# Optimization experiments

Hardware: AMD Instinct MI355X
Metric: run time of the kernel (lower is better)

## Reference

```python
import jax, jax.numpy as jnp
import numpy as np
from functools import partial

C = 10   # number of regular-repr fields
G = 4    # C4 rotation group order
EPS = 1e-5


def _lift_kernel(w):
    """Lifting (trivial->regular) P4 kernel. w: [C, Cin, k, k] ->
    full kernel [C*G, Cin, k, k] with output channel layout (field, orientation)."""
    ks = [jnp.rot90(w, r, axes=(-2, -1)) for r in range(G)]  # each [C,Cin,k,k]
    k = jnp.stack(ks, axis=1)                                 # [C,G,Cin,k,k]
    return k.reshape(w.shape[0] * G, w.shape[1], w.shape[2], w.shape[3])


def _gconv_kernel(w):
    """Regular->regular P4 kernel. w: [Cout, Cin, G, k, k] (indexed by relative
    input orientation) -> full kernel [Cout*G, Cin*G, k, k].
    K[co*G+r, ci*G+s] = rot90(w[co, ci, (s-r) mod G], r)."""
    Cout, Cin, _, k1, k2 = w.shape
    ks = []
    for r in range(G):
        wr = jnp.roll(w, shift=r, axis=2)             # wr[..., s, :, :] = w[..., (s-r)%G]
        wr = jnp.rot90(wr, r, axes=(-2, -1))          # rotate spatially by r*90deg
        ks.append(wr)
    k = jnp.stack(ks, axis=1)                          # [Cout, G, Cin, G, k, k]
    return k.reshape(Cout * G, Cin * G, k1, k2)


def _conv(x, k, pad):
    return jax.lax.conv_general_dilated(
        x, k, window_strides=(1, 1), padding=pad,
        dimension_numbers=('NCHW', 'OIHW', 'NCHW'))


def _bn_relu(x, gamma, beta):
    """InnerBatchNorm (stats shared over the G orientations of each field) + ReLU."""
    B, CG, H, W = x.shape
    xr = x.reshape(B, C, G, H, W)
    m = xr.mean(axis=(0, 2, 3, 4), keepdims=True)
    v = xr.var(axis=(0, 2, 3, 4), keepdims=True)
    g = gamma[None, :, None, None, None]
    b = beta[None, :, None, None, None]
    y = (xr - m) * jax.lax.rsqrt(v + EPS) * g + b
    return jnp.maximum(y.reshape(B, CG, H, W), 0.0)


def _maxpool2(x):
    return jax.lax.reduce_window(x, -jnp.inf, jax.lax.max,
                                 (1, 1, 2, 2), (1, 1, 2, 2), 'VALID')


def setup_inputs() -> dict:
    key = jax.random.key(0)
    ks = jax.random.split(key, 20)
    B = 1024
    x = jax.random.normal(ks[0], (B, 1, 28, 28), dtype=jnp.float32)
    w1 = jax.random.normal(ks[1], (C, 1, 3, 3), dtype=jnp.float32) * 0.3
    w2 = jax.random.normal(ks[2], (C, C, G, 3, 3), dtype=jnp.float32) * 0.1
    w3 = jax.random.normal(ks[3], (C, C, G, 3, 3), dtype=jnp.float32) * 0.1
    w4 = jax.random.normal(ks[4], (C, C, G, 3, 3), dtype=jnp.float32) * 0.1
    w5 = jax.random.normal(ks[5], (C, C, G, 3, 3), dtype=jnp.float32) * 0.1
    w6 = jax.random.normal(ks[6], (C, C, G, 3, 3), dtype=jnp.float32) * 0.1
    w7 = jax.random.normal(ks[7], (C, C, G, 4, 4), dtype=jnp.float32) * 0.1
    g1 = jnp.ones((C,), jnp.float32) + 0.1 * jax.random.normal(ks[8], (C,))
    b1 = 0.1 * jax.random.normal(ks[9], (C,))
    g2 = jnp.ones((C,), jnp.float32) + 0.1 * jax.random.normal(ks[10], (C,))
    b2 = 0.1 * jax.random.normal(ks[11], (C,))
    gs = jnp.ones((C,), jnp.float32) + 0.1 * jax.random.normal(ks[12], (C,))
    bs = 0.1 * jax.random.normal(ks[13], (C,))
    wfc = jax.random.normal(ks[14], (10, C * 11 * 11), dtype=jnp.float32) * 0.05
    bfc = jnp.zeros((10,), jnp.float32)
    return dict(x=x, w1=w1, w2=w2, w3=w3, w4=w4, w5=w5, w6=w6, w7=w7,
                g1=g1, b1=b1, g2=g2, b2=b2, gs=gs, bs=bs, wfc=wfc, bfc=bfc)


PAD1 = [(1, 1), (1, 1)]
PAD0 = [(0, 0), (0, 0)]


def reference(x, w1, w2, w3, w4, w5, w6, w7, g1, b1, g2, b2, gs, bs, wfc, bfc):
    # block1: lifting P4 conv 3x3 pad1 + InnerBN + ReLU  -> [B, 40, 28, 28]
    h = _bn_relu(_conv(x, _lift_kernel(w1), PAD1), g1, b1)
    # block2: P4 conv + BN + ReLU + 2x2 max pool         -> [B, 40, 14, 14]
    h = _maxpool2(_bn_relu(_conv(h, _gconv_kernel(w2), PAD1), g2, b2))
    # blocks 3-6: P4 conv + shared BN/ReLU               -> [B, 40, 14, 14]
    for w in (w3, w4, w5, w6):
        h = _bn_relu(_conv(h, _gconv_kernel(w), PAD1), gs, bs)
    # block7: P4 conv 4x4 pad0 + shared BN/ReLU          -> [B, 40, 11, 11]
    h = _bn_relu(_conv(h, _gconv_kernel(w7), PAD0), gs, bs)
    # group pooling: max over the G orientations of each field -> [B, 10, 11, 11]
    B = h.shape[0]
    h = h.reshape(B, C, G, 11, 11).max(axis=2)
    # fc
    return h.reshape(B, -1) @ wfc.T + bfc
```

## Files before the change

kernel.cpp:

```cpp
#include <hip/hip_runtime.h>

#define EPSV 1e-5f
#define INV28 (1.f / 3211264.f)
#define INV14 (1.f / 802816.f)
#define INV11 (1.f / 495616.f)

typedef _Float16 v8h __attribute__((ext_vector_type(8)));
typedef _Float16 v4h __attribute__((ext_vector_type(4)));
typedef float v4f __attribute__((ext_vector_type(4)));

__device__ __forceinline__ int rotsrc(int r, int dy, int dx, int K) {
  int sy, sx;
  if (r == 0)      { sy = dy;       sx = dx; }
  else if (r == 1) { sy = dx;       sx = K - 1 - dy; }
  else if (r == 2) { sy = K - 1 - dy; sx = K - 1 - dx; }
  else             { sy = K - 1 - dx; sx = dy; }
  return sy * K + sx;
}

__device__ __forceinline__ float gw_val(const float* __restrict__ w, int oc, int g,
                                        int j, int KS) {
  int tap = g / 5, cig = g % 5, ci = cig * 8 + j;
  int co = oc >> 2, r = oc & 3, cin = ci >> 2, s = ci & 3;
  int srel = (s - r) & 3;
  return w[((co * 10 + cin) * 4 + srel) * (KS * KS) + rotsrc(r, tap / KS, tap % KS, KS)];
}

__device__ __forceinline__ float stat8a(const float* __restrict__ p, int i) {
  float v = 0.f;
#pragma unroll
  for (int c = 0; c < 8; ++c)
    v += __hip_atomic_load(&p[c * 32 + i], __ATOMIC_RELAXED, __HIP_MEMORY_SCOPE_AGENT);
  return v;
}

__global__ void prep_kernel(const float* __restrict__ w1, const float* __restrict__ w2,
                            const float* __restrict__ w3, const float* __restrict__ w4,
                            const float* __restrict__ w5, const float* __restrict__ w6,
                            const float* __restrict__ w7,
                            float* __restrict__ K1, _Float16* __restrict__ Wb,
                            float* __restrict__ stats) {
  int idx = blockIdx.x * blockDim.x + threadIdx.x;
  if (idx < 1792) { stats[idx] = 0.f; return; }
  idx -= 1792;
  if (idx < 360) {
    int tap = idx / 40, oc = idx % 40;
    int c = oc >> 2, r = oc & 3;
    K1[idx] = w1[c * 9 + rotsrc(r, tap / 3, tap % 3, 3)];
    return;
  }
  idx -= 360;
  if (idx < 92160) {
    int l = idx / 18432, r0 = idx % 18432;
    const float* w = (l == 0) ? w2 : (l == 1) ? w3 : (l == 2) ? w4 : (l == 3) ? w5 : w6;
    int mt = r0 / 6144, r1 = r0 % 6144;
    int c = r1 / 512, r2 = r1 % 512;
    int q = r2 / 128, r3 = r2 % 128;
    int ocl = r3 / 8, j = r3 % 8;
    int oc = mt * 16 + ocl, g = c * 4 + q;
    float val = 0.f;
    if (oc < 40 && g < 45) val = gw_val(w, oc, g, j, 3);
    Wb[idx] = (_Float16)val;
    return;
  }
  idx -= 92160;
  if (idx < 30720) {
    int mt = idx / 10240, r1 = idx % 10240;
    int c = r1 / 512, r2 = r1 % 512;
    int q = r2 / 128, r3 = r2 % 128;
    int ocl = r3 / 8, j = r3 % 8;
    int oc = mt * 16 + ocl, g = c * 4 + q;
    float val = 0.f;
    if (oc < 40) val = gw_val(w7, oc, g, j, 4);
    Wb[92160 + idx] = (_Float16)val;
    return;
  }
  idx -= 30720;
  if (idx < 1536) {
    int mt = idx / 512, r1 = idx % 512;
    int q = r1 / 128, r2 = r1 % 128;
    int ocl = r2 / 8, j = r2 % 8;
    int oc = mt * 16 + ocl, k = q * 8 + j;
    float val = 0.f;
    if (oc < 40 && k < 9)
      val = w1[(oc >> 2) * 9 + rotsrc(oc & 3, k / 3, k % 3, 3)];
    Wb[122880 + idx] = (_Float16)val;
  }
}

__global__ __launch_bounds__(256) void conv1_stats(
    const float* __restrict__ x, const float* __restrict__ K1,
    float* __restrict__ stats) {
  __shared__ float ximg[900];
  __shared__ float wk[360];
  __shared__ float sstat[20];
  const int tid = threadIdx.x, img = blockIdx.x;
  if (tid < 20) sstat[tid] = 0.f;
  for (int i = tid; i < 900; i += 256) {
    int gy = i / 30 - 1, gx = i % 30 - 1;
    ximg[i] = (gy >= 0 && gy < 28 && gx >= 0 && gx < 28)
                  ? x[img * 784 + gy * 28 + gx] : 0.f;
  }
  for (int i = tid; i < 360; i += 256) wk[i] = K1[i];
  __syncthreads();

  float s[10], q[10];
#pragma unroll
  for (int f = 0; f < 10; ++f) { s[f] = 0.f; q[f] = 0.f; }
  for (int p = tid; p < 784; p += 256) {
    const int y = p / 28, xx = p % 28;
    float patch[9];
#pragma unroll
    for (int t = 0; t < 9; ++t) patch[t] = ximg[(y + t / 3) * 30 + xx + t % 3];
#pragma unroll
    for (int f = 0; f < 10; ++f) {
#pragma unroll
      for (int r = 0; r < 4; ++r) {
        const int oc = f * 4 + r;
        float v = 0.f;
#pragma unroll
        for (int t = 0; t < 9; ++t) v = fmaf(patch[t], wk[t * 40 + oc], v);
        s[f] += v; q[f] += v * v;
      }
    }
  }
#pragma unroll
  for (int f = 0; f < 10; ++f) {
#pragma unroll
    for (int off = 1; off <= 32; off <<= 1) {
      s[f] += __shfl_xor(s[f], off, 64);
      q[f] += __shfl_xor(q[f], off, 64);
    }
  }
  if ((tid & 63) == 0) {
#pragma unroll
    for (int f = 0; f < 10; ++f) {
      atomicAdd(&sstat[f], s[f]);
      atomicAdd(&sstat[10 + f], q[f]);
    }
  }
  __syncthreads();
  if (tid < 20) atomicAdd(&stats[(img & 7) * 32 + tid], sstat[tid]);
}

template<int R>
__global__ __launch_bounds__(256) void conv_band_fused(
    const float* __restrict__ x, const _Float16* __restrict__ W1m,
    const _Float16* __restrict__ Wl, const float* __restrict__ pstats,
    const float* __restrict__ pgamma, const float* __restrict__ pbeta,
    float pinvn, _Float16* __restrict__ T0, float* __restrict__ stats) {
  constexpr int NPIX = R * 28, NSUB = NPIX / 16, NSW = (NSUB + 3) / 4;
  constexpr int SROWS = R + 2, XR = R + 4;
  constexpr int NPIX_S = SROWS * 30, NSUB_S = (NPIX_S + 15) / 16;
  __shared__ __attribute__((aligned(16))) _Float16 tile[SROWS * 30 * 40];
  __shared__ _Float16 xpatch[XR * 32];
  __shared__ float sc[10], sh[10], sstat[20];
  const int tid = threadIdx.x;
  int img, y0;
  if constexpr (R == 8) { img = blockIdx.x / 3; y0 = (blockIdx.x % 3) * 8; }
  else { img = blockIdx.x; y0 = 24; }

  if (tid < 20) sstat[tid] = 0.f;
  if (tid >= 32 && tid < 42) {
    int f = tid - 32;
    float mu = stat8a(pstats, f) * pinvn, q = stat8a(pstats, 10 + f) * pinvn;
    float isd = rsqrtf(q - mu * mu + EPSV);
    float s = pgamma[f] * isd;
    sc[f] = s; sh[f] = pbeta[f] - mu * s;
  }
  for (int i = tid; i < XR * 32; i += 256) {
    int gy = y0 - 2 + i / 32, gx = i % 32 - 2;
    float v = (gy >= 0 && gy < 28 && gx >= 0 && gx < 28)
                  ? x[(long)img * 784 + gy * 28 + gx] : 0.f;
    xpatch[i] = (_Float16)v;
  }
  __syncthreads();

  const int lane = tid & 63, wv = tid >> 6;
  const int m = lane & 15, quad = lane >> 4;

  {
    v8h a1[3];
#pragma unroll
    for (int mt = 0; mt < 3; ++mt)
      a1[mt] = *(const v8h*)(W1m + mt * 512 + (quad * 16 + m) * 8);
    for (int ns = wv; ns < NSUB_S; ns += 4) {
      const int n = ns * 16 + m;
      const bool valid = n < NPIX_S;
      const int nc = valid ? n : NPIX_S - 1;
      const int iy = nc / 30, ix = nc % 30;
      v8h bfr;
#pragma unroll
      for (int j = 0; j < 8; ++j) bfr[j] = (_Float16)0.f;
      if (quad < 2) {
#pragma unroll
        for (int j = 0; j < 8; ++j) {
          const int k = quad * 8 + j;
          if (k < 9) bfr[j] = xpatch[(iy + k / 3) * 32 + (ix + k % 3)];
        }
      }
      v4f cfr[3];
#pragma unroll
      for (int mt = 0; mt < 3; ++mt)
        cfr[mt] = __builtin_amdgcn_mfma_f32_16x16x32_f16(
            a1[mt], bfr, (v4f){0.f, 0.f, 0.f, 0.f}, 0, 0, 0);
      const int gy = y0 + iy - 1, gx = ix - 1;
      const bool inb = (gy >= 0 && gy < 28 && gx >= 0 && gx < 28);
#pragma unroll
      for (int mt = 0; mt < 3; ++mt) {
        if (mt == 2 && quad >= 2) continue;
        const int f = mt * 4 + quad;
        const float scf = sc[f], shf = sh[f];
        v4h pk;
#pragma unroll
        for (int r = 0; r < 4; ++r) {
          float v = inb ? fmaxf(0.f, fmaf(cfr[mt][r], scf, shf)) : 0.f;
          pk[r] = (_Float16)v;
        }
        if (valid) *(v4h*)&tile[nc * 40 + mt * 16 + quad * 4] = pk;
      }
    }
  }
  __syncthreads();

  int pbase[NSW], nsv[NSW];
  bool sv[NSW];
#pragma unroll
  for (int s = 0; s < NSW; ++s) {
    int ns = wv + 4 * s;
    sv[s] = ns < NSUB;
    int n = ns * 16 + m;
    n = n < NPIX ? n : NPIX - 1;
    nsv[s] = n;
    pbase[s] = ((n / 28) * 30 + (n % 28)) * 40;
  }
  v4f acc[3][NSW] = {};

  const _Float16* wlane = Wl + (quad * 16 + m) * 8;
  for (int c = 0; c < 12; ++c) {
    int g = 4 * c + quad; g = g > 44 ? 44 : g;
    int tap = g / 5, cig = g - tap * 5;
    int boff = ((tap / 3) * 30 + (tap % 3)) * 40 + cig * 8;
    v8h bfr[NSW];
#pragma unroll
    for (int s = 0; s < NSW; ++s)
      if (sv[s]) bfr[s] = *(const v8h*)&tile[pbase[s] + boff];
    v8h afr[3];
#pragma unroll
    for (int mt = 0; mt < 3; ++mt)
      afr[mt] = *(const v8h*)(wlane + (mt * 12 + c) * 512);
#pragma unroll
    for (int s = 0; s < NSW; ++s)
      if (sv[s]) {
#pragma unroll
        for (int mt = 0; mt < 3; ++mt)
          acc[mt][s] = __builtin_amdgcn_mfma_f32_16x16x32_f16(afr[mt], bfr[s],
                                                             acc[mt][s], 0, 0, 0);
      }
  }

#pragma unroll
  for (int mt = 0; mt < 3; ++mt) {
    float svv = 0.f, qvv = 0.f;
#pragma unroll
    for (int s = 0; s < NSW; ++s)
      if (sv[s]) {
#pragma unroll
        for (int r = 0; r < 4; ++r) { float v = acc[mt][s][r]; svv += v; qvv += v * v; }
      }
    const bool ocok = (mt < 2) || (quad < 2);
#pragma unroll
    for (int off = 1; off <= 8; off <<= 1) {
      svv += __shfl_xor(svv, off, 64);
      qvv += __shfl_xor(qvv, off, 64);
    }
    if (m == 0 && ocok) {
      atomicAdd(&sstat[mt * 4 + quad], svv);
      atomicAdd(&sstat[10 + mt * 4 + quad], qvv);
    }
  }

  __syncthreads();
  _Float16* pool = tile;
#pragma unroll
  for (int mt = 0; mt < 3; ++mt) {
    const bool ocok = (mt < 2) || (quad < 2);
    const int oc0 = mt * 16 + quad * 4;
#pragma unroll
    for (int s = 0; s < NSW; ++s)
      if (ocok && sv[s]) {
#pragma unroll
        for (int r = 0; r < 4; ++r)
          pool[(oc0 + r) * NPIX + nsv[s]] = (_Float16)acc[mt][s][r];
      }
  }
  __syncthreads();
  constexpr int PR = R / 2, PCNT = 40 * PR * 14;
  for (int i = tid; i < PCNT; i += 256) {
    int oc = i / (PR * 14), rem = i % (PR * 14);
    int py = rem / 14, px = rem % 14;
    const _Float16* pp = pool + oc * NPIX + py * 56 + px * 2;
    float a = (float)pp[0], b = (float)pp[1], c = (float)pp[28], d = (float)pp[29];
    T0[((long)img * 256 + (y0 / 2 + py + 1) * 16 + (px + 1)) * 40 + oc] =
        (_Float16)fmaxf(fmaxf(a, b), fmaxf(c, d));
  }
  if (tid < 20) atomicAdd(&stats[(img & 7) * 32 + tid], sstat[tid]);
}

__global__ __launch_bounds__(256) void conv_tile(
    const _Float16* __restrict__ Tin, const _Float16* __restrict__ Wl,
    const float* __restrict__ pstats, const float* __restrict__ pg,
    const float* __restrict__ pb, float pinvn,
    _Float16* __restrict__ Tout, float* __restrict__ stG) {
  __shared__ __attribute__((aligned(16))) _Float16 tile[256 * 40];
  __shared__ float sc[10], sh[10], sstat[20];
  const int tid = threadIdx.x, img = blockIdx.x;
  const int lane = tid & 63, wv = tid >> 6;
  const int m = lane & 15, quad = lane >> 4;
  if (tid < 20) sstat[tid] = 0.f;
  if (tid >= 32 && tid < 42) {
    int f = tid - 32;
    float mu = stat8a(pstats, f) * pinvn, q = stat8a(pstats, 10 + f) * pinvn;
    float isd = rsqrtf(q - mu * mu + EPSV);
    float s = pg[f] * isd;
    sc[f] = s; sh[f] = pb[f] - mu * s;
  }
  __syncthreads();
  {
    const int iy = tid >> 4, ix = tid & 15;
    const bool border = (iy == 0) | (iy == 15) | (ix == 0) | (ix == 15);
    const _Float16* src = Tin + ((long)img * 256 + tid) * 40;
    _Float16* dst = &tile[tid * 40];
#pragma unroll
    for (int cg5 = 0; cg5 < 5; ++cg5) {
      v8h pk;
      if (!border) {
        v8h rv = *(const v8h*)(src + cg5 * 8);
#pragma unroll
        for (int u = 0; u < 8; ++u) {
          const int f = (cg5 * 8 + u) >> 2;
          pk[u] = (_Float16)fmaxf(0.f, fmaf((float)rv[u], sc[f], sh[f]));
        }
      } else {
#pragma unroll
        for (int u = 0; u < 8; ++u) pk[u] = (_Float16)0.f;
      }
      *(v8h*)(dst + cg5 * 8) = pk;
    }
  }
  __syncthreads();

  int pb3[4], n3[4];
  bool sv3[4], va3[4];
#pragma unroll
  for (int s = 0; s < 4; ++s) {
    int ns = wv + 4 * s;
    sv3[s] = ns < 13;
    int n = ns * 16 + m;
    va3[s] = sv3[s] && (n < 196);
    n = n < 196 ? n : 195;
    n3[s] = n;
    pb3[s] = ((n / 14) * 16 + (n % 14)) * 40;
  }
  const int wofs = (quad * 16 + m) * 8;
  v4f acc[3][4];
#pragma unroll
  for (int mt = 0; mt < 3; ++mt)
#pragma unroll
    for (int s = 0; s < 4; ++s) acc[mt][s] = (v4f){0.f, 0.f, 0.f, 0.f};
  for (int c = 0; c < 12; ++c) {
    int g = 4 * c + quad; g = g > 44 ? 44 : g;
    int tap = g / 5, cig = g - tap * 5;
    int boff = ((tap / 3) * 16 + (tap % 3)) * 40 + cig * 8;
    v8h bfr[4];
#pragma unroll
    for (int s = 0; s < 4; ++s)
      if (sv3[s]) bfr[s] = *(const v8h*)&tile[pb3[s] + boff];
    v8h afr[3];
#pragma unroll
    for (int mt = 0; mt < 3; ++mt)
      afr[mt] = *(const v8h*)(Wl + wofs + (mt * 12 + c) * 512);
#pragma unroll
    for (int s = 0; s < 4; ++s)
      if (sv3[s]) {
#pragma unroll
        for (int mt = 0; mt < 3; ++mt)
          acc[mt][s] = __builtin_amdgcn_mfma_f32_16x16x32_f16(afr[mt], bfr[s],
                                                             acc[mt][s], 0, 0, 0);
      }
  }

#pragma unroll
  for (int mt = 0; mt < 3; ++mt) {
    float svv = 0.f, qvv = 0.f;
#pragma unroll
    for (int s = 0; s < 4; ++s)
      if (va3[s]) {
#pragma unroll
        for (int r = 0; r < 4; ++r) { float v = acc[mt][s][r]; svv += v; qvv += v * v; }
      }
    const bool ocok = (mt < 2) || (quad < 2);
#pragma unroll
    for (int off = 1; off <= 8; off <<= 1) {
      svv += __shfl_xor(svv, off, 64);
      qvv += __shfl_xor(qvv, off, 64);
    }
    if (m == 0 && ocok) {
      atomicAdd(&sstat[mt * 4 + quad], svv);
      atomicAdd(&sstat[10 + mt * 4 + quad], qvv);
    }
  }
  __syncthreads();
  if (tid < 20) atomicAdd(&stG[(img & 7) * 32 + tid], sstat[tid]);

#pragma unroll
  for (int mt = 0; mt < 3; ++mt) {
    const bool ocok = (mt < 2) || (quad < 2);
    if (!ocok) continue;
#pragma unroll
    for (int s = 0; s < 4; ++s)
      if (va3[s]) {
        v4h pk;
#pragma unroll
        for (int r = 0; r < 4; ++r) pk[r] = (_Float16)acc[mt][s][r];
        const int n = n3[s];
        *(v4h*)(Tout + ((long)img * 256 + (n / 14 + 1) * 16 + (n % 14 + 1)) * 40
                + mt * 16 + quad * 4) = pk;
      }
  }
}

__global__ __launch_bounds__(256) void conv7_tile(
    const _Float16* __restrict__ Tin, const _Float16* __restrict__ Wl,
    const float* __restrict__ pstats, const float* __restrict__ pg,
    const float* __restrict__ pb,
    _Float16* __restrict__ T7, float* __restrict__ stG) {
  __shared__ __attribute__((aligned(16))) _Float16 tile[256 * 40];
  __shared__ float sc[10], sh[10], sstat[20];
  const int tid = threadIdx.x, img = blockIdx.x;
  const int lane = tid & 63, wv = tid >> 6;
  const int m = lane & 15, quad = lane >> 4;
  if (tid < 20) sstat[tid] = 0.f;
  if (tid >= 32 && tid < 42) {
    int f = tid - 32;
    float mu = stat8a(pstats, f) * INV14, q = stat8a(pstats, 10 + f) * INV14;
    float isd = rsqrtf(q - mu * mu + EPSV);
    float s = pg[f] * isd;
    sc[f] = s; sh[f] = pb[f] - mu * s;
  }
  __syncthreads();
  {
    const int iy = tid >> 4, ix = tid & 15;
    const bool border = (iy == 0) | (iy == 15) | (ix == 0) | (ix == 15);
    const _Float16* src = Tin + ((long)img * 256 + tid) * 40;
    _Float16* dst = &tile[tid * 40];
#pragma unroll
    for (int cg5 = 0; cg5 < 5; ++cg5) {
      v8h pk;
      if (!border) {
        v8h rv = *(const v8h*)(src + cg5 * 8);
#pragma unroll
        for (int u = 0; u < 8; ++u) {
          const int f = (cg5 * 8 + u) >> 2;
          pk[u] = (_Float16)fmaxf(0.f, fmaf((float)rv[u], sc[f], sh[f]));
        }
      } else {
#pragma unroll
        for (int u = 0; u < 8; ++u) pk[u] = (_Float16)0.f;
      }
      *(v8h*)(dst + cg5 * 8) = pk;
    }
  }
  __syncthreads();

  int pb7[2], n7[2];
  bool va7[2];
#pragma unroll
  for (int s = 0; s < 2; ++s) {
    int ns = wv + 4 * s;
    int n = ns * 16 + m;
    va7[s] = n < 121;
    n = n < 121 ? n : 120;
    n7[s] = n;
    pb7[s] = ((n / 11 + 1) * 16 + (n % 11 + 1)) * 40;
  }
  const int wofs = (quad * 16 + m) * 8;
  v4f acc[3][2];
#pragma unroll
  for (int mt = 0; mt < 3; ++mt)
#pragma unroll
    for (int s = 0; s < 2; ++s) acc[mt][s] = (v4f){0.f, 0.f, 0.f, 0.f};
  for (int c = 0; c < 20; ++c) {
    int g = 4 * c + quad;
    int tap = g / 5, cig = g - tap * 5;
    int boff = ((tap >> 2) * 16 + (tap & 3)) * 40 + cig * 8;
    v8h bfr[2];
#pragma unroll
    for (int s = 0; s < 2; ++s) bfr[s] = *(const v8h*)&tile[pb7[s] + boff];
    v8h afr[3];
#pragma unroll
    for (int mt = 0; mt < 3; ++mt)
      afr[mt] = *(const v8h*)(Wl + wofs + (mt * 20 + c) * 512);
#pragma unroll
    for (int s = 0; s < 2; ++s)
#pragma unroll
      for (int mt = 0; mt < 3; ++mt)
        acc[mt][s] = __builtin_amdgcn_mfma_f32_16x16x32_f16(afr[mt], bfr[s],
                                                           acc[mt][s], 0, 0, 0);
  }

#pragma unroll
  for (int mt = 0; mt < 3; ++mt) {
    float svv = 0.f, qvv = 0.f;
#pragma unroll
    for (int s = 0; s < 2; ++s)
      if (va7[s]) {
#pragma unroll
        for (int r = 0; r < 4; ++r) { float v = acc[mt][s][r]; svv += v; qvv += v * v; }
      }
    const bool ocok = (mt < 2) || (quad < 2);
#pragma unroll
    for (int off = 1; off <= 8; off <<= 1) {
      svv += __shfl_xor(svv, off, 64);
      qvv += __shfl_xor(qvv, off, 64);
    }
    if (m == 0 && ocok) {
      atomicAdd(&sstat[mt * 4 + quad], svv);
      atomicAdd(&sstat[10 + mt * 4 + quad], qvv);
    }
  }
  __syncthreads();
  if (tid < 20) atomicAdd(&stG[(img & 7) * 32 + tid], sstat[tid]);

#pragma unroll
  for (int mt = 0; mt < 3; ++mt) {
    const bool ocok = (mt < 2) || (quad < 2);
    if (!ocok) continue;
#pragma unroll
    for (int s = 0; s < 2; ++s)
      if (va7[s]) {
        v4h pk;
#pragma unroll
        for (int r = 0; r < 4; ++r) pk[r] = (_Float16)acc[mt][s][r];
        *(v4h*)(T7 + ((long)img * 121 + n7[s]) * 40 + mt * 16 + quad * 4) = pk;
      }
  }
}

__global__ __launch_bounds__(256) void head_kernel(
    const _Float16* __restrict__ T7, const float* __restrict__ stats7,
    const float* __restrict__ gs, const float* __restrict__ bs,
    const float* __restrict__ wfc, const float* __restrict__ bfc,
    float* __restrict__ out) {
  __shared__ float sc[10], sh[10];
  __shared__ float mbuf[1210];
  __shared__ float red[40];
  const int tid = threadIdx.x, img = blockIdx.x;
  if (tid < 10) {
    float mu = stat8a(stats7, tid) * INV11, q = stat8a(stats7, 10 + tid) * INV11;
    float isd = rsqrtf(q - mu * mu + EPSV);
    float s = gs[tid] * isd;
    sc[tid] = s;
    sh[tid] = bs[tid] - mu * s;
  }
  __syncthreads();
  for (int p = tid; p < 121; p += 256) {
    const _Float16* rp = T7 + ((long)img * 121 + p) * 40;
#pragma unroll
    for (int cg5 = 0; cg5 < 5; ++cg5) {
      v8h v = *(const v8h*)(rp + cg5 * 8);
#pragma unroll
      for (int fh = 0; fh < 2; ++fh) {
        const int f = cg5 * 2 + fh;
        float mx = fmaf((float)v[fh * 4], sc[f], sh[f]);
#pragma unroll
        for (int r = 1; r < 4; ++r)
          mx = fmaxf(mx, fmaf((float)v[fh * 4 + r], sc[f], sh[f]));
        mbuf[f * 121 + p] = fmaxf(0.f, mx);
      }
    }
  }
  __syncthreads();
  const int wv = tid >> 6;
  for (int k = 0; k < 10; ++k) {
    float p = 0.f;
    for (int j = tid; j < 1210; j += 256) p = fmaf(mbuf[j], wfc[k * 1210 + j], p);
#pragma unroll
    for (int off = 32; off > 0; off >>= 1) p += __shfl_xor(p, off, 64);
    if ((tid & 63) == 0) red[k * 4 + wv] = p;
  }
  __syncthreads();
  if (tid < 10)
    out[img * 10 + tid] = bfc[tid] + red[tid * 4] + red[tid * 4 + 1] +
                          red[tid * 4 + 2] + red[tid * 4 + 3];
}

extern "C" void kernel_launch(void* const* d_in, const int* in_sizes, int n_in,
                              void* d_out, int out_size, void* d_ws, size_t ws_size,
                              hipStream_t stream) {
  const float* x   = (const float*)d_in[0];
  const float* w1  = (const float*)d_in[1];
  const float* w2  = (const float*)d_in[2];
  const float* w3  = (const float*)d_in[3];
  const float* w4  = (const float*)d_in[4];
  const float* w5  = (const float*)d_in[5];
  const float* w6  = (const float*)d_in[6];
  const float* w7  = (const float*)d_in[7];
  const float* g1  = (const float*)d_in[8];
  const float* b1  = (const float*)d_in[9];
  const float* g2  = (const float*)d_in[10];
  const float* b2  = (const float*)d_in[11];
  const float* gs  = (const float*)d_in[12];
  const float* bs  = (const float*)d_in[13];
  const float* wfc = (const float*)d_in[14];
  const float* bfc = (const float*)d_in[15];

  float* ws = (float*)d_ws;
  float* K1      = ws;
  float* stats   = ws + 360;
  _Float16* Wb   = (_Float16*)(ws + 2152);
  _Float16* W1m  = Wb + 122880;
  _Float16* T0   = (_Float16*)(ws + 64360);
  _Float16* T1   = (_Float16*)(ws + 5307240L);
  _Float16* T7   = (_Float16*)(ws + 10550120L);

  prep_kernel<<<495, 256, 0, stream>>>(w1, w2, w3, w4, w5, w6, w7, K1, Wb, stats);
  conv1_stats<<<1024, 256, 0, stream>>>(x, K1, stats);
  conv_band_fused<8><<<3072, 256, 0, stream>>>(x, W1m, Wb, stats, g1, b1, INV28,
                                               T0, stats + 256);
  conv_band_fused<4><<<1024, 256, 0, stream>>>(x, W1m, Wb, stats, g1, b1, INV28,
                                               T0, stats + 256);
  conv_tile<<<1024, 256, 0, stream>>>(T0, Wb + 18432, stats + 256, g2, b2, INV28,
                                      T1, stats + 512);
  conv_tile<<<1024, 256, 0, stream>>>(T1, Wb + 36864, stats + 512, gs, bs, INV14,
                                      T0, stats + 768);
  conv_tile<<<1024, 256, 0, stream>>>(T0, Wb + 55296, stats + 768, gs, bs, INV14,
                                      T1, stats + 1024);
  conv_tile<<<1024, 256, 0, stream>>>(T1, Wb + 73728, stats + 1024, gs, bs, INV14,
                                      T0, stats + 1280);
  conv7_tile<<<1024, 256, 0, stream>>>(T0, Wb + 92160, stats + 1280, gs, bs,
                                       T7, stats + 1536);
  head_kernel<<<1024, 256, 0, stream>>>(T7, stats + 1536, gs, bs, wfc, bfc,
                                        (float*)d_out);
}
```

Baseline: 321.4 us.

## Merge band conv kernels into one launch and precompute im2col patches

The two template instances of the fused block-2 band convolution (8-row and 4-row bands) become a single kernel launched once with 4096 blocks, where each block works out its band height at runtime. An im2col buffer of the 3x3 input patches is built in shared memory, so the first-layer MFMA operand is one vector load instead of eight scalar gathers. This removes one kernel launch and its tail. In exchange, band sizes are no longer compile-time constants, the accumulator arrays are sized for the largest case, and shared memory use and register pressure rise.

```diff
diff --git a/kernel.cpp b/kernel.cpp
--- a/kernel.cpp
+++ b/kernel.cpp
@@ -143,22 +143,23 @@
   if (tid < 20) atomicAdd(&stats[(img & 7) * 32 + tid], sstat[tid]);
 }
 
-template<int R>
-__global__ __launch_bounds__(256) void conv_band_fused(
+__global__ __launch_bounds__(256) void conv_band_all(
     const float* __restrict__ x, const _Float16* __restrict__ W1m,
     const _Float16* __restrict__ Wl, const float* __restrict__ pstats,
     const float* __restrict__ pgamma, const float* __restrict__ pbeta,
     float pinvn, _Float16* __restrict__ T0, float* __restrict__ stats) {
-  constexpr int NPIX = R * 28, NSUB = NPIX / 16, NSW = (NSUB + 3) / 4;
-  constexpr int SROWS = R + 2, XR = R + 4;
-  constexpr int NPIX_S = SROWS * 30, NSUB_S = (NPIX_S + 15) / 16;
-  __shared__ __attribute__((aligned(16))) _Float16 tile[SROWS * 30 * 40];
-  __shared__ _Float16 xpatch[XR * 32];
+  __shared__ __attribute__((aligned(16))) _Float16 tile[300 * 40];
+  __shared__ __attribute__((aligned(16))) _Float16 xcol[300 * 8];
+  __shared__ _Float16 xpatch[12 * 32];
   __shared__ float sc[10], sh[10], sstat[20];
   const int tid = threadIdx.x;
-  int img, y0;
-  if constexpr (R == 8) { img = blockIdx.x / 3; y0 = (blockIdx.x % 3) * 8; }
-  else { img = blockIdx.x; y0 = 24; }
+  const int img = blockIdx.x >> 2, slot = blockIdx.x & 3;
+  const int R = (slot < 3) ? 8 : 4;
+  const int y0 = (slot < 3) ? slot * 8 : 24;
+  const int npix = R * 28, nsub = npix >> 4;
+  const int srows = R + 2, npix_s = srows * 30;
+  const int nsub_s = (npix_s + 15) >> 4;
+  const int xr = R + 4;
 
   if (tid < 20) sstat[tid] = 0.f;
   if (tid >= 32 && tid < 42) {
@@ -168,7 +169,7 @@
     float s = pgamma[f] * isd;
     sc[f] = s; sh[f] = pbeta[f] - mu * s;
   }
-  for (int i = tid; i < XR * 32; i += 256) {
+  for (int i = tid; i < xr * 32; i += 256) {
     int gy = y0 - 2 + i / 32, gx = i % 32 - 2;
     float v = (gy >= 0 && gy < 28 && gx >= 0 && gx < 28)
                   ? x[(long)img * 784 + gy * 28 + gx] : 0.f;
@@ -176,6 +177,16 @@
   }
   __syncthreads();
 
+  for (int p = tid; p < npix_s; p += 256) {
+    const int iy = p / 30, ix = p % 30;
+    v8h c0;
+#pragma unroll
+    for (int j = 0; j < 8; ++j)
+      c0[j] = xpatch[(iy + j / 3) * 32 + ix + j % 3];
+    *(v8h*)&xcol[p * 8] = c0;
+  }
+  __syncthreads();
+
   const int lane = tid & 63, wv = tid >> 6;
   const int m = lane & 15, quad = lane >> 4;
 
@@ -184,21 +195,16 @@
 #pragma unroll
     for (int mt = 0; mt < 3; ++mt)
       a1[mt] = *(const v8h*)(W1m + mt * 512 + (quad * 16 + m) * 8);
-    for (int ns = wv; ns < NSUB_S; ns += 4) {
+    for (int ns = wv; ns < nsub_s; ns += 4) {
       const int n = ns * 16 + m;
-      const bool valid = n < NPIX_S;
-      const int nc = valid ? n : NPIX_S - 1;
+      const bool valid = n < npix_s;
+      const int nc = valid ? n : npix_s - 1;
       const int iy = nc / 30, ix = nc % 30;
       v8h bfr;
 #pragma unroll
       for (int j = 0; j < 8; ++j) bfr[j] = (_Float16)0.f;
-      if (quad < 2) {
-#pragma unroll
-        for (int j = 0; j < 8; ++j) {
-          const int k = quad * 8 + j;
-          if (k < 9) bfr[j] = xpatch[(iy + k / 3) * 32 + (ix + k % 3)];
-        }
-      }
+      if (quad == 0) bfr = *(const v8h*)&xcol[nc * 8];
+      else if (quad == 1) bfr[0] = xpatch[(iy + 2) * 32 + ix + 2];
       v4f cfr[3];
 #pragma unroll
       for (int mt = 0; mt < 3; ++mt)
@@ -223,34 +229,34 @@
   }
   __syncthreads();
 
-  int pbase[NSW], nsv[NSW];
-  bool sv[NSW];
-#pragma unroll
-  for (int s = 0; s < NSW; ++s) {
+  int pbase[4], nsv[4];
+  bool sv[4];
+#pragma unroll
+  for (int s = 0; s < 4; ++s) {
     int ns = wv + 4 * s;
-    sv[s] = ns < NSUB;
+    sv[s] = ns < nsub;
     int n = ns * 16 + m;
-    n = n < NPIX ? n : NPIX - 1;
+    n = n < npix ? n : npix - 1;
     nsv[s] = n;
     pbase[s] = ((n / 28) * 30 + (n % 28)) * 40;
   }
-  v4f acc[3][NSW] = {};
+  v4f acc[3][4] = {};
 
   const _Float16* wlane = Wl + (quad * 16 + m) * 8;
   for (int c = 0; c < 12; ++c) {
     int g = 4 * c + quad; g = g > 44 ? 44 : g;
     int tap = g / 5, cig = g - tap * 5;
     int boff = ((tap / 3) * 30 + (tap % 3)) * 40 + cig * 8;
-    v8h bfr[NSW];
-#pragma unroll
-    for (int s = 0; s < NSW; ++s)
+    v8h bfr[4];
+#pragma unroll
+    for (int s = 0; s < 4; ++s)
       if (sv[s]) bfr[s] = *(const v8h*)&tile[pbase[s] + boff];
     v8h afr[3];
 #pragma unroll
     for (int mt = 0; mt < 3; ++mt)
       afr[mt] = *(const v8h*)(wlane + (mt * 12 + c) * 512);
 #pragma unroll
-    for (int s = 0; s < NSW; ++s)
+    for (int s = 0; s < 4; ++s)
       if (sv[s]) {
 #pragma unroll
         for (int mt = 0; mt < 3; ++mt)
@@ -263,7 +269,7 @@
   for (int mt = 0; mt < 3; ++mt) {
     float svv = 0.f, qvv = 0.f;
 #pragma unroll
-    for (int s = 0; s < NSW; ++s)
+    for (int s = 0; s < 4; ++s)
       if (sv[s]) {
 #pragma unroll
         for (int r = 0; r < 4; ++r) { float v = acc[mt][s][r]; svv += v; qvv += v * v; }
@@ -287,19 +293,19 @@
     const bool ocok = (mt < 2) || (quad < 2);
     const int oc0 = mt * 16 + quad * 4;
 #pragma unroll
-    for (int s = 0; s < NSW; ++s)
+    for (int s = 0; s < 4; ++s)
       if (ocok && sv[s]) {
 #pragma unroll
         for (int r = 0; r < 4; ++r)
-          pool[(oc0 + r) * NPIX + nsv[s]] = (_Float16)acc[mt][s][r];
-      }
-  }
-  __syncthreads();
-  constexpr int PR = R / 2, PCNT = 40 * PR * 14;
-  for (int i = tid; i < PCNT; i += 256) {
-    int oc = i / (PR * 14), rem = i % (PR * 14);
+          pool[(oc0 + r) * npix + nsv[s]] = (_Float16)acc[mt][s][r];
+      }
+  }
+  __syncthreads();
+  const int pr = R / 2, pcnt = 40 * pr * 14;
+  for (int i = tid; i < pcnt; i += 256) {
+    int oc = i / (pr * 14), rem = i % (pr * 14);
     int py = rem / 14, px = rem % 14;
-    const _Float16* pp = pool + oc * NPIX + py * 56 + px * 2;
+    const _Float16* pp = pool + oc * npix + py * 56 + px * 2;
     float a = (float)pp[0], b = (float)pp[1], c = (float)pp[28], d = (float)pp[29];
     T0[((long)img * 256 + (y0 / 2 + py + 1) * 16 + (px + 1)) * 40 + oc] =
         (_Float16)fmaxf(fmaxf(a, b), fmaxf(c, d));
@@ -626,10 +632,8 @@
 
   prep_kernel<<<495, 256, 0, stream>>>(w1, w2, w3, w4, w5, w6, w7, K1, Wb, stats);
   conv1_stats<<<1024, 256, 0, stream>>>(x, K1, stats);
-  conv_band_fused<8><<<3072, 256, 0, stream>>>(x, W1m, Wb, stats, g1, b1, INV28,
-                                               T0, stats + 256);
-  conv_band_fused<4><<<1024, 256, 0, stream>>>(x, W1m, Wb, stats, g1, b1, INV28,
-                                               T0, stats + 256);
+  conv_band_all<<<4096, 256, 0, stream>>>(x, W1m, Wb, stats, g1, b1, INV28,
+                                          T0, stats + 256);
   conv_tile<<<1024, 256, 0, stream>>>(T0, Wb + 18432, stats + 256, g2, b2, INV28,
                                       T1, stats + 512);
   conv_tile<<<1024, 256, 0, stream>>>(T1, Wb + 36864, stats + 512, gs, bs, INV14,
```

Result: no change. 322.9 us (+0.5%).
